# Performance work log

Measured on AMD Instinct MI355X. Metric: run time of the kernel, lower is better.

## Reference

```python
import jax, jax.numpy as jnp
import numpy as np

RESIDUAL_SCALE = 0.002

def setup_inputs() -> dict:
    key = jax.random.key(0)
    x = jax.random.normal(key, (8, 128, 64, 64), dtype=jnp.float32)
    return {"x": x}

def reference(x):
    b, c, w, h = x.shape
    f = x.reshape(b, c, w * h)                      # [b, c, wh]
    # scores[b,i,j] = sum_c x[b,c,i] * x[b,c,j]  (hvi @ gui)
    scores = jnp.einsum('bci,bcj->bij', f, f)       # [b, wh, wh]
    # torch F.softmax(UiVi, 1): softmax over the first wh axis (axis=1)
    attn = jax.nn.softmax(scores, axis=1)
    # Ai = lui @ attn_map -> [b, c, wh]
    ai = jnp.einsum('bci,bij->bcj', f, attn)
    return x + RESIDUAL_SCALE * ai.reshape(b, c, w, h)
```

## Files before the change

kernel.cpp:

```cpp
#include <hip/hip_runtime.h>


typedef __bf16 bf16;
typedef bf16 bf16x4 __attribute__((ext_vector_type(4)));
typedef bf16 bf16x8 __attribute__((ext_vector_type(8)));
typedef float f32x4 __attribute__((ext_vector_type(4)));

#define BATCH 8
#define CD 128
#define NN 4096
#define QBLK 64
#define KVB 64
#define NT (NN / KVB)

#define KT_BY(row, colb) (((row) << 8) + ((colb) ^ (((row) & 7) << 4)))
#define VT_BY(row, colb) (((row) << 7) + ((colb) ^ (((row) & 7) << 4)))
#define PT_BY(row, colb) (((row) << 7) + ((colb) ^ (((row) & 7) << 4)))

__global__ __launch_bounds__(256) void transpose_to_bf16(const float* __restrict__ x,
                                                         bf16* __restrict__ ft) {
    __shared__ float tile[32][33];
    const int n0 = blockIdx.x * 32;
    const int c0 = blockIdx.y * 32;
    const int b  = blockIdx.z;
    const int tx = threadIdx.x & 7;
    const int ty = threadIdx.x >> 3;

    f32x4 v = *reinterpret_cast<const f32x4*>(
        x + ((size_t)b * CD + c0 + ty) * NN + n0 + tx * 4);
#pragma unroll
    for (int e = 0; e < 4; e++) tile[ty][tx * 4 + e] = v[e];
    __syncthreads();

    bf16x4 o;
#pragma unroll
    for (int e = 0; e < 4; e++) o[e] = (bf16)tile[tx * 4 + e][ty];
    *reinterpret_cast<bf16x4*>(
        ft + ((size_t)b * NN + n0 + ty) * CD + c0 + tx * 4) = o;
}

__global__ __launch_bounds__(256, 2) void attn_kernel(const float* __restrict__ x,
                                                      const bf16* __restrict__ ft,
                                                      float* __restrict__ out) {
    const int tid = threadIdx.x;
    const int w   = tid >> 6;
    const int l   = tid & 63;
    const int l15 = l & 15;
    const int l4  = l >> 4;
    const int l15b4 = (l15 & 7) << 4;

    const int batch = blockIdx.x >> 6;
    const int q0    = (blockIdx.x & 63) * QBLK;

    const bf16*  ftb = ft + (size_t)batch * NN * CD;
    const float* xb  = x  + (size_t)batch * CD * NN;

    __shared__ union {
        struct {
            bf16 kt[2][KVB][128];
            bf16 vt[2][CD][64];
            bf16 p[4][16][64];
        } s;
        float o[QBLK][CD + 5];
    } sm;

    bf16x8 qf[4];
    {
        const bf16* qrow = ftb + (size_t)(q0 + w * 16 + l15) * CD + l4 * 8;
#pragma unroll
        for (int ct = 0; ct < 4; ct++)
            qf[ct] = *reinterpret_cast<const bf16x8*>(qrow + ct * 32);
    }

    const int srow = tid >> 4;
    const int sch  = tid & 15;

    bf16x8 kreg[4];
    f32x4  vreg[8];

    auto stage_load = [&](int i0) {
#pragma unroll
        for (int j = 0; j < 4; j++)
            kreg[j] = *reinterpret_cast<const bf16x8*>(
                ftb + (size_t)(i0 + j * 16 + srow) * CD + sch * 8);
#pragma unroll
        for (int j = 0; j < 8; j++)
            vreg[j] = *reinterpret_cast<const f32x4*>(
                xb + (size_t)(j * 16 + srow) * NN + i0 + sch * 4);
    };
    auto stage_write = [&](int buf) {
        char* ktb = (char*)sm.s.kt[buf];
        char* vtb = (char*)sm.s.vt[buf];
#pragma unroll
        for (int j = 0; j < 4; j++)
            *reinterpret_cast<bf16x8*>(ktb + KT_BY(j * 16 + srow, sch * 16)) = kreg[j];
#pragma unroll
        for (int j = 0; j < 8; j++) {
            bf16x4 t;
#pragma unroll
            for (int e = 0; e < 4; e++) t[e] = (bf16)vreg[j][e];
            *reinterpret_cast<bf16x4*>(vtb + VT_BY(j * 16 + srow, sch * 8)) = t;
        }
    };

    const f32x4 zero = {0.0f, 0.0f, 0.0f, 0.0f};
    f32x4 oacc[8];
#pragma unroll
    for (int i = 0; i < 8; i++) oacc[i] = zero;
    float m_run = -1e30f;
    float l_par = 0.0f;

    stage_load(0);
    stage_write(0);
    __syncthreads();

    for (int it = 0; it < NT; ++it) {
        const int cur = it & 1;
        if (it + 1 < NT) stage_load((it + 1) * KVB);

        const char* ktb = (const char*)sm.s.kt[cur];
        const char* vtb = (const char*)sm.s.vt[cur];
        char*       pb  = (char*)sm.s.p[w];

        f32x4 s[4];
        __builtin_amdgcn_s_setprio(1);
#pragma unroll
        for (int g = 0; g < 4; g++) {
            s[g] = zero;
#pragma unroll
            for (int ct = 0; ct < 4; ct++) {
                bf16x8 kf = *reinterpret_cast<const bf16x8*>(
                    ktb + KT_BY(g * 16 + l15, ct * 64 + l4 * 16));
                s[g] = __builtin_amdgcn_mfma_f32_16x16x32_bf16(kf, qf[ct], s[g], 0, 0, 0);
            }
        }
        __builtin_amdgcn_s_setprio(0);

        float mp;
        {
            float m0 = fmaxf(fmaxf(s[0][0], s[0][1]), fmaxf(s[0][2], s[0][3]));
            float m1 = fmaxf(fmaxf(s[1][0], s[1][1]), fmaxf(s[1][2], s[1][3]));
            float m2 = fmaxf(fmaxf(s[2][0], s[2][1]), fmaxf(s[2][2], s[2][3]));
            float m3 = fmaxf(fmaxf(s[3][0], s[3][1]), fmaxf(s[3][2], s[3][3]));
            mp = fmaxf(fmaxf(m0, m1), fmaxf(m2, m3));
        }
        mp = fmaxf(mp, __shfl_xor(mp, 16));
        mp = fmaxf(mp, __shfl_xor(mp, 32));

        if (__any(mp > m_run + 8.0f)) {
            const float mn    = fmaxf(m_run, mp);
            const float alpha = __expf(m_run - mn);
            m_run = mn;
            l_par *= alpha;
            float a[4];
#pragma unroll
            for (int r = 0; r < 4; r++) a[r] = __shfl(alpha, l4 * 4 + r);
#pragma unroll
            for (int ct = 0; ct < 8; ct++)
#pragma unroll
                for (int r = 0; r < 4; r++) oacc[ct][r] *= a[r];
        }

        float pe[4][4];
        float ps = 0.0f;
#pragma unroll
        for (int g = 0; g < 4; g++)
#pragma unroll
            for (int r = 0; r < 4; r++) {
                pe[g][r] = __expf(s[g][r] - m_run);
                ps += pe[g][r];
            }
        l_par += ps;

#pragma unroll
        for (int g = 0; g < 4; g++) {
            bf16x4 t;
#pragma unroll
            for (int r = 0; r < 4; r++) t[r] = (bf16)pe[g][r];
            *reinterpret_cast<bf16x4*>(pb + (((int)l15 << 7) +
                ((g * 32 + l4 * 8) ^ l15b4))) = t;
        }
        bf16x8 pf0 = *reinterpret_cast<const bf16x8*>(
            pb + (((int)l15 << 7) + ((l4 * 16) ^ l15b4)));
        bf16x8 pf1 = *reinterpret_cast<const bf16x8*>(
            pb + (((int)l15 << 7) + ((64 + l4 * 16) ^ l15b4)));

        __builtin_amdgcn_s_setprio(1);
#pragma unroll
        for (int ct = 0; ct < 8; ct++) {
            bf16x8 vf0 = *reinterpret_cast<const bf16x8*>(
                vtb + VT_BY(ct * 16 + l15, l4 * 16));
            bf16x8 vf1 = *reinterpret_cast<const bf16x8*>(
                vtb + VT_BY(ct * 16 + l15, 64 + l4 * 16));
            oacc[ct] = __builtin_amdgcn_mfma_f32_16x16x32_bf16(pf0, vf0, oacc[ct], 0, 0, 0);
            oacc[ct] = __builtin_amdgcn_mfma_f32_16x16x32_bf16(pf1, vf1, oacc[ct], 0, 0, 0);
        }
        __builtin_amdgcn_s_setprio(0);

        if (it + 1 < NT) stage_write(cur ^ 1);
        __syncthreads();
    }

    float L = l_par;
    L += __shfl_xor(L, 16);
    L += __shfl_xor(L, 32);
    float rl[4];
#pragma unroll
    for (int r = 0; r < 4; r++) rl[r] = 1.0f / __shfl(L, l4 * 4 + r);

#pragma unroll
    for (int r = 0; r < 4; r++)
#pragma unroll
        for (int ct = 0; ct < 8; ct++)
            sm.o[w * 16 + l4 * 4 + r][ct * 16 + l15] = oacc[ct][r] * rl[r];
    __syncthreads();

    const size_t xbase = (size_t)batch * CD * NN;
    for (int idx = tid; idx < QBLK * CD; idx += 256) {
        const int c = idx >> 6;
        const int q = idx & 63;
        const size_t g = xbase + (size_t)c * NN + q0 + q;
        out[g] = x[g] + 0.002f * sm.o[q][c];
    }
}

extern "C" void kernel_launch(void* const* d_in, const int* in_sizes, int n_in,
                              void* d_out, int out_size, void* d_ws, size_t ws_size,
                              hipStream_t stream) {
    const float* x = (const float*)d_in[0];
    float* out = (float*)d_out;
    bf16* ft = (bf16*)d_ws;

    dim3 tb1(256);
    dim3 tg1(NN / 32, CD / 32, BATCH);
    transpose_to_bf16<<<tg1, tb1, 0, stream>>>(x, ft);

    attn_kernel<<<512, 256, 0, stream>>>(x, ft, out);
}
```

Before: 185.9 us.

## Switch attention to 32x32 MFMA with split-KV waves and register P exchange

The attention kernel now uses 32x32x16 bf16 MFMAs with 128-query blocks and 512 threads. The 8 waves split each KV tile into two halves and merge the partial softmax states at the end. P is passed between lanes with shuffles instead of an LDS round trip, Q is prescaled by log2e so exp2 can be used, and the epilogue stores vectorised f32x4. The transpose kernel is replaced by a gather with no LDS, and the grid is interleaved across batches. The aims are higher MFMA efficiency and fewer LDS and exp costs. The trade-offs are 256 blocks on a large GPU, higher register pressure, and a looser rescale threshold.

Result: faster. 178.4 us (-4.0%).

```diff
diff --git a/kernel.cpp b/kernel.cpp
--- a/kernel.cpp
+++ b/kernel.cpp
@@ -2,111 +2,120 @@
 
 
 typedef __bf16 bf16;
+typedef bf16 bf16x2 __attribute__((ext_vector_type(2)));
 typedef bf16 bf16x4 __attribute__((ext_vector_type(4)));
 typedef bf16 bf16x8 __attribute__((ext_vector_type(8)));
 typedef float f32x4 __attribute__((ext_vector_type(4)));
+typedef float f32x16 __attribute__((ext_vector_type(16)));
+typedef unsigned int u32;
+typedef u32 u32x4 __attribute__((ext_vector_type(4)));
 
 #define BATCH 8
 #define CD 128
 #define NN 4096
-#define QBLK 64
+#define QBLK 128
 #define KVB 64
 #define NT (NN / KVB)
+#define LOG2E 1.44269504f
 
 #define KT_BY(row, colb) (((row) << 8) + ((colb) ^ (((row) & 7) << 4)))
 #define VT_BY(row, colb) (((row) << 7) + ((colb) ^ (((row) & 7) << 4)))
-#define PT_BY(row, colb) (((row) << 7) + ((colb) ^ (((row) & 7) << 4)))
 
 __global__ __launch_bounds__(256) void transpose_to_bf16(const float* __restrict__ x,
                                                          bf16* __restrict__ ft) {
-    __shared__ float tile[32][33];
-    const int n0 = blockIdx.x * 32;
-    const int c0 = blockIdx.y * 32;
-    const int b  = blockIdx.z;
-    const int tx = threadIdx.x & 7;
-    const int ty = threadIdx.x >> 3;
-
-    f32x4 v = *reinterpret_cast<const f32x4*>(
-        x + ((size_t)b * CD + c0 + ty) * NN + n0 + tx * 4);
-#pragma unroll
-    for (int e = 0; e < 4; e++) tile[ty][tx * 4 + e] = v[e];
-    __syncthreads();
-
-    bf16x4 o;
-#pragma unroll
-    for (int e = 0; e < 4; e++) o[e] = (bf16)tile[tx * 4 + e][ty];
-    *reinterpret_cast<bf16x4*>(
-        ft + ((size_t)b * NN + n0 + ty) * CD + c0 + tx * 4) = o;
+    const u32 g  = blockIdx.x * 256 + threadIdx.x;
+    const u32 b  = g >> 16;
+    const u32 r  = g & 65535;
+    const u32 n_lo  = r & 15;
+    const u32 c8_lo = (r >> 4) & 3;
+    const u32 hi    = r >> 6;
+    const u32 c8 = (hi & 3) * 4 + c8_lo;
+    const u32 n  = (hi >> 2) * 16 + n_lo;
+    const float* xb = x + (size_t)b * CD * NN;
+    bf16x8 o;
+#pragma unroll
+    for (int e = 0; e < 8; e++)
+        o[e] = (bf16)xb[(size_t)(c8 * 8 + e) * NN + n];
+    *reinterpret_cast<bf16x8*>(ft + ((size_t)b * NN + n) * CD + c8 * 8) = o;
 }
 
-__global__ __launch_bounds__(256, 2) void attn_kernel(const float* __restrict__ x,
+__global__ __launch_bounds__(512, 2) void attn_kernel(const float* __restrict__ x,
                                                       const bf16* __restrict__ ft,
                                                       float* __restrict__ out) {
     const int tid = threadIdx.x;
     const int w   = tid >> 6;
+    const int wq  = w & 3;
+    const int wk  = w >> 2;
     const int l   = tid & 63;
-    const int l15 = l & 15;
-    const int l4  = l >> 4;
-    const int l15b4 = (l15 & 7) << 4;
-
-    const int batch = blockIdx.x >> 6;
-    const int q0    = (blockIdx.x & 63) * QBLK;
-
-    const bf16*  ftb = ft + (size_t)batch * NN * CD;
-    const float* xb  = x  + (size_t)batch * CD * NN;
+    const int l31 = l & 31;
+    const int h   = l >> 5;
+
+    const int batch = blockIdx.x & 7;
+    const int q0    = (blockIdx.x >> 3) * QBLK;
+
+    const bf16*  ftb  = ft  + (size_t)batch * NN * CD;
+    const float* xb   = x   + (size_t)batch * CD * NN;
+    float*       outb = out + (size_t)batch * CD * NN;
 
     __shared__ union {
         struct {
-            bf16 kt[2][KVB][128];
-            bf16 vt[2][CD][64];
-            bf16 p[4][16][64];
+            bf16 kt[2][KVB * 128];
+            bf16 vt[2][CD * 64];
         } s;
-        float o[QBLK][CD + 5];
+        float o[QBLK][133];
     } sm;
-
-    bf16x8 qf[4];
+    __shared__ float s_mx[8][32], s_ls[8][32];
+
+    bf16x8 qf[8];
     {
-        const bf16* qrow = ftb + (size_t)(q0 + w * 16 + l15) * CD + l4 * 8;
-#pragma unroll
-        for (int ct = 0; ct < 4; ct++)
-            qf[ct] = *reinterpret_cast<const bf16x8*>(qrow + ct * 32);
-    }
-
-    const int srow = tid >> 4;
-    const int sch  = tid & 15;
-
-    bf16x8 kreg[4];
-    f32x4  vreg[8];
-
+        const bf16* qp = ftb + (size_t)(q0 + wq * 32 + l31) * CD + h * 8;
+#pragma unroll
+        for (int kst = 0; kst < 8; kst++) {
+            bf16x8 t = *reinterpret_cast<const bf16x8*>(qp + kst * 16);
+#pragma unroll
+            for (int e = 0; e < 8; e++) qf[kst][e] = (bf16)((float)t[e] * LOG2E);
+        }
+    }
+
+    bf16x8 kreg[2];
+    f32x4  vreg[4];
     auto stage_load = [&](int i0) {
 #pragma unroll
-        for (int j = 0; j < 4; j++)
+        for (int j = 0; j < 2; j++) {
+            const int slot = tid + j * 512;
             kreg[j] = *reinterpret_cast<const bf16x8*>(
-                ftb + (size_t)(i0 + j * 16 + srow) * CD + sch * 8);
-#pragma unroll
-        for (int j = 0; j < 8; j++)
+                ftb + (size_t)(i0 + (slot >> 4)) * CD + (slot & 15) * 8);
+        }
+#pragma unroll
+        for (int j = 0; j < 4; j++) {
+            const int slot = tid + j * 512;
             vreg[j] = *reinterpret_cast<const f32x4*>(
-                xb + (size_t)(j * 16 + srow) * NN + i0 + sch * 4);
+                xb + (size_t)(slot >> 4) * NN + i0 + (slot & 15) * 4);
+        }
     };
     auto stage_write = [&](int buf) {
         char* ktb = (char*)sm.s.kt[buf];
         char* vtb = (char*)sm.s.vt[buf];
 #pragma unroll
-        for (int j = 0; j < 4; j++)
-            *reinterpret_cast<bf16x8*>(ktb + KT_BY(j * 16 + srow, sch * 16)) = kreg[j];
-#pragma unroll
-        for (int j = 0; j < 8; j++) {
+        for (int j = 0; j < 2; j++) {
+            const int slot = tid + j * 512;
+            *reinterpret_cast<bf16x8*>(ktb + KT_BY(slot >> 4, (slot & 15) * 16)) = kreg[j];
+        }
+#pragma unroll
+        for (int j = 0; j < 4; j++) {
+            const int slot = tid + j * 512;
             bf16x4 t;
 #pragma unroll
             for (int e = 0; e < 4; e++) t[e] = (bf16)vreg[j][e];
-            *reinterpret_cast<bf16x4*>(vtb + VT_BY(j * 16 + srow, sch * 8)) = t;
+            *reinterpret_cast<bf16x4*>(vtb + VT_BY(slot >> 4, (slot & 15) * 8)) = t;
         }
     };
 
-    const f32x4 zero = {0.0f, 0.0f, 0.0f, 0.0f};
-    f32x4 oacc[8];
-#pragma unroll
-    for (int i = 0; i < 8; i++) oacc[i] = zero;
+    f32x16 oacc[4];
+#pragma unroll
+    for (int ct = 0; ct < 4; ct++)
+#pragma unroll
+        for (int r = 0; r < 16; r++) oacc[ct][r] = 0.0f;
     float m_run = -1e30f;
     float l_par = 0.0f;
 
@@ -120,80 +129,73 @@
 
         const char* ktb = (const char*)sm.s.kt[cur];
         const char* vtb = (const char*)sm.s.vt[cur];
-        char*       pb  = (char*)sm.s.p[w];
-
-        f32x4 s[4];
+
+        f32x16 sA, sB;
+#pragma unroll
+        for (int r = 0; r < 16; r++) { sA[r] = 0.0f; sB[r] = 0.0f; }
         __builtin_amdgcn_s_setprio(1);
 #pragma unroll
-        for (int g = 0; g < 4; g++) {
-            s[g] = zero;
-#pragma unroll
-            for (int ct = 0; ct < 4; ct++) {
-                bf16x8 kf = *reinterpret_cast<const bf16x8*>(
-                    ktb + KT_BY(g * 16 + l15, ct * 64 + l4 * 16));
-                s[g] = __builtin_amdgcn_mfma_f32_16x16x32_bf16(kf, qf[ct], s[g], 0, 0, 0);
+        for (int kst = 0; kst < 8; kst += 2) {
+            bf16x8 kf0 = *reinterpret_cast<const bf16x8*>(
+                ktb + KT_BY(wk * 32 + l31, kst * 32 + h * 16));
+            bf16x8 kf1 = *reinterpret_cast<const bf16x8*>(
+                ktb + KT_BY(wk * 32 + l31, (kst + 1) * 32 + h * 16));
+            sA = __builtin_amdgcn_mfma_f32_32x32x16_bf16(kf0, qf[kst], sA, 0, 0, 0);
+            sB = __builtin_amdgcn_mfma_f32_32x32x16_bf16(kf1, qf[kst + 1], sB, 0, 0, 0);
+        }
+        __builtin_amdgcn_s_setprio(0);
+        float s[16];
+#pragma unroll
+        for (int r = 0; r < 16; r++) s[r] = sA[r] + sB[r];
+
+        float mp = s[0];
+#pragma unroll
+        for (int r = 1; r < 16; r++) mp = fmaxf(mp, s[r]);
+        mp = fmaxf(mp, __shfl_xor(mp, 32));
+
+        if (__any(mp > m_run + 11.5f)) {
+            const float mn = fmaxf(m_run, mp);
+            const float al = exp2f(m_run - mn);
+            m_run = mn;
+            l_par *= al;
+#pragma unroll
+            for (int ct = 0; ct < 4; ct++)
+#pragma unroll
+                for (int r = 0; r < 16; r++) oacc[ct][r] *= al;
+        }
+
+        float pe[16];
+        float ps = 0.0f;
+#pragma unroll
+        for (int r = 0; r < 16; r++) { pe[r] = exp2f(s[r] - m_run); ps += pe[r]; }
+        l_par += ps;
+
+        u32 W[4][2], Xs[4][2];
+#pragma unroll
+        for (int gg = 0; gg < 4; gg++)
+#pragma unroll
+            for (int j = 0; j < 2; j++) {
+                bf16x2 t = {(bf16)pe[4 * gg + 2 * j], (bf16)pe[4 * gg + 2 * j + 1]};
+                W[gg][j] = __builtin_bit_cast(unsigned short, t[0]) |
+                           ((u32)__builtin_bit_cast(unsigned short, t[1]) << 16);
+                Xs[gg][j] = (u32)__shfl_xor((int)W[gg][j], 32);
             }
-        }
-        __builtin_amdgcn_s_setprio(0);
-
-        float mp;
-        {
-            float m0 = fmaxf(fmaxf(s[0][0], s[0][1]), fmaxf(s[0][2], s[0][3]));
-            float m1 = fmaxf(fmaxf(s[1][0], s[1][1]), fmaxf(s[1][2], s[1][3]));
-            float m2 = fmaxf(fmaxf(s[2][0], s[2][1]), fmaxf(s[2][2], s[2][3]));
-            float m3 = fmaxf(fmaxf(s[3][0], s[3][1]), fmaxf(s[3][2], s[3][3]));
-            mp = fmaxf(fmaxf(m0, m1), fmaxf(m2, m3));
-        }
-        mp = fmaxf(mp, __shfl_xor(mp, 16));
-        mp = fmaxf(mp, __shfl_xor(mp, 32));
-
-        if (__any(mp > m_run + 8.0f)) {
-            const float mn    = fmaxf(m_run, mp);
-            const float alpha = __expf(m_run - mn);
-            m_run = mn;
-            l_par *= alpha;
-            float a[4];
-#pragma unroll
-            for (int r = 0; r < 4; r++) a[r] = __shfl(alpha, l4 * 4 + r);
-#pragma unroll
-            for (int ct = 0; ct < 8; ct++)
-#pragma unroll
-                for (int r = 0; r < 4; r++) oacc[ct][r] *= a[r];
-        }
-
-        float pe[4][4];
-        float ps = 0.0f;
-#pragma unroll
-        for (int g = 0; g < 4; g++)
-#pragma unroll
-            for (int r = 0; r < 4; r++) {
-                pe[g][r] = __expf(s[g][r] - m_run);
-                ps += pe[g][r];
-            }
-        l_par += ps;
-
-#pragma unroll
-        for (int g = 0; g < 4; g++) {
-            bf16x4 t;
-#pragma unroll
-            for (int r = 0; r < 4; r++) t[r] = (bf16)pe[g][r];
-            *reinterpret_cast<bf16x4*>(pb + (((int)l15 << 7) +
-                ((g * 32 + l4 * 8) ^ l15b4))) = t;
-        }
-        bf16x8 pf0 = *reinterpret_cast<const bf16x8*>(
-            pb + (((int)l15 << 7) + ((l4 * 16) ^ l15b4)));
-        bf16x8 pf1 = *reinterpret_cast<const bf16x8*>(
-            pb + (((int)l15 << 7) + ((64 + l4 * 16) ^ l15b4)));
+        u32x4 pw0 = {h ? Xs[1][0] : W[0][0], h ? Xs[1][1] : W[0][1],
+                     h ? W[1][0] : Xs[0][0], h ? W[1][1] : Xs[0][1]};
+        u32x4 pw1 = {h ? Xs[3][0] : W[2][0], h ? Xs[3][1] : W[2][1],
+                     h ? W[3][0] : Xs[2][0], h ? W[3][1] : Xs[2][1]};
+        bf16x8 pa0 = __builtin_bit_cast(bf16x8, pw0);
+        bf16x8 pa1 = __builtin_bit_cast(bf16x8, pw1);
 
         __builtin_amdgcn_s_setprio(1);
 #pragma unroll
-        for (int ct = 0; ct < 8; ct++) {
+        for (int ct = 0; ct < 4; ct++) {
             bf16x8 vf0 = *reinterpret_cast<const bf16x8*>(
-                vtb + VT_BY(ct * 16 + l15, l4 * 16));
+                vtb + VT_BY(ct * 32 + l31, wk * 64 + h * 16));
+            oacc[ct] = __builtin_amdgcn_mfma_f32_32x32x16_bf16(pa0, vf0, oacc[ct], 0, 0, 0);
             bf16x8 vf1 = *reinterpret_cast<const bf16x8*>(
-                vtb + VT_BY(ct * 16 + l15, 64 + l4 * 16));
-            oacc[ct] = __builtin_amdgcn_mfma_f32_16x16x32_bf16(pf0, vf0, oacc[ct], 0, 0, 0);
-            oacc[ct] = __builtin_amdgcn_mfma_f32_16x16x32_bf16(pf1, vf1, oacc[ct], 0, 0, 0);
+                vtb + VT_BY(ct * 32 + l31, wk * 64 + 32 + h * 16));
+            oacc[ct] = __builtin_amdgcn_mfma_f32_32x32x16_bf16(pa1, vf1, oacc[ct], 0, 0, 0);
         }
         __builtin_amdgcn_s_setprio(0);
 
@@ -201,26 +203,46 @@
         __syncthreads();
     }
 
-    float L = l_par;
-    L += __shfl_xor(L, 16);
-    L += __shfl_xor(L, 32);
-    float rl[4];
-#pragma unroll
-    for (int r = 0; r < 4; r++) rl[r] = 1.0f / __shfl(L, l4 * 4 + r);
-
-#pragma unroll
-    for (int r = 0; r < 4; r++)
-#pragma unroll
-        for (int ct = 0; ct < 8; ct++)
-            sm.o[w * 16 + l4 * 4 + r][ct * 16 + l15] = oacc[ct][r] * rl[r];
-    __syncthreads();
-
-    const size_t xbase = (size_t)batch * CD * NN;
-    for (int idx = tid; idx < QBLK * CD; idx += 256) {
-        const int c = idx >> 6;
-        const int q = idx & 63;
-        const size_t g = xbase + (size_t)c * NN + q0 + q;
-        out[g] = x[g] + 0.002f * sm.o[q][c];
+    const float L = l_par + __shfl_xor(l_par, 32);
+    if (l < 32) { s_mx[w][l31] = m_run; s_ls[w][l31] = L; }
+    __syncthreads();
+    const float m_o = s_mx[w ^ 4][l31];
+    const float L_o = s_ls[w ^ 4][l31];
+    const float m_p = fmaxf(m_run, m_o);
+    const float eS  = exp2f(m_run - m_p);
+    const float eO  = exp2f(m_o - m_p);
+    const float fsc = eS / (L * eS + L_o * eO);
+
+    if (wk == 0) {
+#pragma unroll
+        for (int ct = 0; ct < 4; ct++)
+#pragma unroll
+            for (int r = 0; r < 16; r++)
+                sm.o[wq * 32 + l31][ct * 32 + (r & 3) + 8 * (r >> 2) + 4 * h] =
+                    oacc[ct][r] * fsc;
+    }
+    __syncthreads();
+    if (wk == 1) {
+#pragma unroll
+        for (int ct = 0; ct < 4; ct++)
+#pragma unroll
+            for (int r = 0; r < 16; r++)
+                sm.o[wq * 32 + l31][ct * 32 + (r & 3) + 8 * (r >> 2) + 4 * h] +=
+                    oacc[ct][r] * fsc;
+    }
+    __syncthreads();
+
+#pragma unroll
+    for (int k = 0; k < 8; k++) {
+        const int slot = tid + k * 512;
+        const int c  = slot >> 5;
+        const int q4 = (slot & 31) * 4;
+        f32x4 xv = *reinterpret_cast<const f32x4*>(xb + (size_t)c * NN + q0 + q4);
+        f32x4 ov;
+#pragma unroll
+        for (int e = 0; e < 4; e++)
+            ov[e] = xv[e] + 0.002f * sm.o[q4 + e][c];
+        *reinterpret_cast<f32x4*>(outb + (size_t)c * NN + q0 + q4) = ov;
     }
 }
 
@@ -231,9 +253,6 @@
     float* out = (float*)d_out;
     bf16* ft = (bf16*)d_ws;
 
-    dim3 tb1(256);
-    dim3 tg1(NN / 32, CD / 32, BATCH);
-    transpose_to_bf16<<<tg1, tb1, 0, stream>>>(x, ft);
-
-    attn_kernel<<<512, 256, 0, stream>>>(x, ft, out);
+    transpose_to_bf16<<<2048, 256, 0, stream>>>(x, ft);
+    attn_kernel<<<256, 512, 0, stream>>>(x, ft, out);
 }
```
